# Kernel optimization log

Measured on AMD Instinct MI355X. Metric: run time of the kernel, lower is better.

## Reference

```python
import jax, jax.numpy as jnp
import numpy as np

D_MODEL = 1024
NUM_HEADS = 16
HEAD_DIM = D_MODEL // NUM_HEADS  # 64
MAX_REL = 512
NUM_EMB = 2 * MAX_REL + 1  # 1025
B, L = 2, 2048


def _glorot(key, shape):
    fan_in, fan_out = shape[0], shape[1]
    lim = jnp.sqrt(6.0 / (fan_in + fan_out))
    return jax.random.uniform(key, shape, jnp.float32, -lim, lim)


def setup_inputs() -> dict:
    key = jax.random.key(0)
    ks = jax.random.split(key, 9)
    return {
        "query": jax.random.normal(ks[0], (B, L, D_MODEL), jnp.float32),
        "key": jax.random.normal(ks[1], (B, L, D_MODEL), jnp.float32),
        "value": jax.random.normal(ks[2], (B, L, D_MODEL), jnp.float32),
        "wq": _glorot(ks[3], (D_MODEL, D_MODEL)), "bq": jnp.zeros((D_MODEL,), jnp.float32),
        "wk": _glorot(ks[4], (D_MODEL, D_MODEL)), "bk": jnp.zeros((D_MODEL,), jnp.float32),
        "wv": _glorot(ks[5], (D_MODEL, D_MODEL)), "bv": jnp.zeros((D_MODEL,), jnp.float32),
        "wo": _glorot(ks[6], (D_MODEL, D_MODEL)), "bo": jnp.zeros((D_MODEL,), jnp.float32),
        "rel_emb": _glorot(ks[7], (NUM_EMB, HEAD_DIM)),
    }


def _split_heads(x):
    b, l, _ = x.shape
    return x.reshape(b, l, NUM_HEADS, HEAD_DIM).transpose(0, 2, 1, 3)  # (b,h,l,d)


def reference(query, key, value, wq, bq, wk, bk, wv, bv, wo, bo, rel_emb):
    q = _split_heads(query @ wq + bq)  # (b,h,l,d)
    k = _split_heads(key @ wk + bk)
    v = _split_heads(value @ wv + bv)

    # content scores: (b,h,l,l)
    content = jnp.einsum('bhid,bhjd->bhij', q, k)

    # relative position scores. Original gathers E[clip(j-i)] -> (L,L,d) then
    # einsum('bhid,ijd->bhij'). Equivalent & cheaper: project q onto all
    # relative embeddings once, then gather along the relative-index axis.
    idx = jnp.arange(q.shape[2])
    final_mat = jnp.clip(idx[None, :] - idx[:, None], -MAX_REL, MAX_REL) + MAX_REL  # (L,L)
    q_rel = jnp.einsum('bhid,rd->bhir', q, rel_emb)  # (b,h,l,num_emb)
    position = jnp.take_along_axis(q_rel, final_mat[None, None, :, :], axis=-1)  # (b,h,l,l)

    scores = (content + position) / jnp.sqrt(jnp.float32(HEAD_DIM))
    weights = jax.nn.softmax(scores, axis=-1)  # no mask, dropout off (inference)
    out = jnp.einsum('bhij,bhjd->bhid', weights, v)  # (b,h,l,d)

    out = out.transpose(0, 2, 1, 3).reshape(query.shape[0], -1, D_MODEL)
    return out @ wo + bo
```

## Files before the change

kernel.cpp:

```cpp
#include <hip/hip_runtime.h>
#include <hip/hip_bf16.h>


typedef __attribute__((ext_vector_type(8))) short short8;
typedef __attribute__((ext_vector_type(4))) float floatx4;

#define L_SEQ 2048
#define D_MODEL 1024
#define NHEAD 16
#define DH 64
#define BH 32
#define MROWS 4096

__device__ inline float b2f(short s) {
    unsigned int u = ((unsigned int)(unsigned short)s) << 16;
    float f; __builtin_memcpy(&f, &u, 4); return f;
}
__device__ inline short f2b(float f) {
    unsigned int u; __builtin_memcpy(&u, &f, 4);
    u += 0x7fffu + ((u >> 16) & 1u);
    return (short)(u >> 16);
}
__device__ inline unsigned int pack2(float a, float b) {
    __hip_bfloat162 h = __float22bfloat162_rn(make_float2(a, b));
    unsigned int u; __builtin_memcpy(&u, &h, 4); return u;
}
__device__ inline void st2(short* p, unsigned int v) {
    __builtin_memcpy(p, &v, 4);
}
__device__ inline void async_cp16(short* lds, const short* g) {
    __builtin_amdgcn_global_load_lds(
        (const __attribute__((address_space(1))) unsigned int*)g,
        (__attribute__((address_space(3))) unsigned int*)lds, 16, 0, 0);
}

__global__ __launch_bounds__(256) void detect_dtype(
        const unsigned short* __restrict__ q, int* __restrict__ flag) {
    __shared__ int s[256];
    int tid = threadIdx.x, cnt = 0;
    for (int i = tid; i < 65536; i += 256)
        if ((q[i] & 0x7F80u) == 0x7F80u) cnt++;
    s[tid] = cnt; __syncthreads();
    for (int st = 128; st; st >>= 1) {
        if (tid < st) s[tid] += s[tid + st];
        __syncthreads();
    }
    if (tid == 0) *flag = (s[0] > 4) ? 1 : 0;
}

__global__ __launch_bounds__(256) void norm_small(
        const void* __restrict__ bq, const void* __restrict__ bk,
        const void* __restrict__ bv, const void* __restrict__ bo,
        const void* __restrict__ rel, float* __restrict__ bias4,
        short* __restrict__ relb, const int* __restrict__ flagp) {
    const int f32 = *flagp;
    int t = blockIdx.x * 256 + threadIdx.x;
    if (t < 4096) {
        const void* src = (t < 1024) ? bq : (t < 2048) ? bk : (t < 3072) ? bv : bo;
        int i = t & 1023;
        bias4[t] = f32 ? ((const float*)src)[i] : b2f(((const short*)src)[i]);
    } else if (t < 4096 + 65600) {
        int i = t - 4096;
        relb[i] = f32 ? f2b(((const float*)rel)[i]) : ((const short*)rel)[i];
    }
}

__global__ __launch_bounds__(256) void transpose4(
        const void* __restrict__ w0, const void* __restrict__ w1,
        const void* __restrict__ w2, const void* __restrict__ w3,
        short* __restrict__ dst, const int* __restrict__ flagp) {
    const int f32 = *flagp;
    __shared__ short tile[32][33];
    const void* src = (blockIdx.z == 0) ? w0 : (blockIdx.z == 1) ? w1
                    : (blockIdx.z == 2) ? w2 : w3;
    short* d = dst + (size_t)blockIdx.z * (D_MODEL * D_MODEL);
    int x = blockIdx.x * 32 + threadIdx.x;
    int y0 = blockIdx.y * 32;
    for (int yy = threadIdx.y; yy < 32; yy += 8) {
        size_t idx = (size_t)(y0 + yy) * D_MODEL + x;
        tile[yy][threadIdx.x] = f32 ? f2b(((const float*)src)[idx])
                                    : ((const short*)src)[idx];
    }
    __syncthreads();
    int x0 = blockIdx.x * 32;
    for (int yy = threadIdx.y; yy < 32; yy += 8)
        d[(size_t)(x0 + yy) * D_MODEL + y0 + threadIdx.x] = tile[threadIdx.x][yy];
}

__global__ __launch_bounds__(256) void proj_gemm(
        const void* __restrict__ Aq, const void* __restrict__ Ak,
        const void* __restrict__ Av, const short* __restrict__ WT,
        const float* __restrict__ bias4, short* __restrict__ Qout,
        const int* __restrict__ flagp) {
    const int f32 = *flagp;
    const int z = blockIdx.z;
    const void* A_ = (z == 0) ? Aq : (z == 1) ? Ak : Av;
    const short* BT = WT + (size_t)z * (D_MODEL * D_MODEL);
    const float* bias = bias4 + z * 1024;
    short* C = Qout + (size_t)z * ((size_t)MROWS * D_MODEL);
    const int K = D_MODEL;

    __shared__ short Alds[128 * 32];
    __shared__ short Blds[128 * 32];
    const int tid = threadIdx.x;
    const int w = tid >> 6, lane = tid & 63, cl = lane & 15, quad = lane >> 4;
    const int wr = w >> 1, wc = w & 1;
    const int m0 = blockIdx.y * 128, n0 = blockIdx.x * 128;
    const int srow = tid >> 2, scol = (tid & 3) * 8;
    const int grow = lane >> 2, gcol = (lane & 3) * 8;

    floatx4 acc[4][4];
    for (int i = 0; i < 4; i++)
        for (int j = 0; j < 4; j++)
            acc[i][j] = {0.f, 0.f, 0.f, 0.f};

    for (int k0 = 0; k0 < K; k0 += 32) {
        for (int s = 0; s < 2; s++) {
            int r = w * 32 + s * 16;
            async_cp16(&Blds[r * 32], &BT[(size_t)(n0 + r + grow) * K + k0 + gcol]);
        }
        if (f32) {
            const float* Af = (const float*)A_;
            for (int half = 0; half < 2; half++) {
                size_t base = (size_t)(m0 + srow + half * 64) * K + k0 + scol;
                float4 f0 = *(const float4*)(&Af[base]);
                float4 f1 = *(const float4*)(&Af[base + 4]);
                uint4 s;
                s.x = pack2(f0.x, f0.y); s.y = pack2(f0.z, f0.w);
                s.z = pack2(f1.x, f1.y); s.w = pack2(f1.z, f1.w);
                *(uint4*)(&Alds[(srow + half * 64) * 32 + scol]) = s;
            }
        } else {
            const short* Ab = (const short*)A_;
            for (int s = 0; s < 2; s++) {
                int r = w * 32 + s * 16;
                async_cp16(&Alds[r * 32], &Ab[(size_t)(m0 + r + grow) * K + k0 + gcol]);
            }
        }
        __syncthreads();

        short8 af[4], bfr[4];
        for (int mt = 0; mt < 4; mt++)
            af[mt] = *(const short8*)(&Alds[(wr * 64 + mt * 16 + cl) * 32 + quad * 8]);
        for (int nt = 0; nt < 4; nt++)
            bfr[nt] = *(const short8*)(&Blds[(wc * 64 + nt * 16 + cl) * 32 + quad * 8]);
        for (int mt = 0; mt < 4; mt++)
            for (int nt = 0; nt < 4; nt++)
                acc[mt][nt] = __builtin_amdgcn_mfma_f32_16x16x32_bf16(
                    af[mt], bfr[nt], acc[mt][nt], 0, 0, 0);
        __syncthreads();
    }

    for (int nt = 0; nt < 4; nt++) {
        int n = n0 + wc * 64 + nt * 16 + cl;
        float bv = bias[n];
        int h = n >> 6, d = n & 63;
        for (int mt = 0; mt < 4; mt++) {
            for (int r = 0; r < 4; r++) {
                int m = m0 + wr * 64 + mt * 16 + quad * 4 + r;
                float v = acc[mt][nt][r] + bv;
                int b = m >> 11, i = m & 2047;
                if (z < 2)
                    C[(((size_t)(b * NHEAD + h)) * L_SEQ + i) * DH + d] = f2b(v);
                else
                    C[(((size_t)(b * NHEAD + h)) * DH + d) * L_SEQ + i] = f2b(v);
            }
        }
    }
}

__global__ __launch_bounds__(256) void out_gemm(
        const short* __restrict__ A, const short* __restrict__ BT,
        const float* __restrict__ bias, void* __restrict__ C_,
        const int* __restrict__ flagp) {
    const int f32 = *flagp;
    const int K = D_MODEL, N = D_MODEL;
    __shared__ short Alds[128 * 32];
    __shared__ short Blds[64 * 32];
    const int tid = threadIdx.x;
    const int w = tid >> 6, lane = tid & 63, cl = lane & 15, quad = lane >> 4;
    const int wr = w >> 1, wc = w & 1;
    const int m0 = blockIdx.y * 128, n0 = blockIdx.x * 64;
    const int grow = lane >> 2, gcol = (lane & 3) * 8;

    floatx4 acc[4][2];
    for (int i = 0; i < 4; i++)
        for (int j = 0; j < 2; j++)
            acc[i][j] = {0.f, 0.f, 0.f, 0.f};

    for (int k0 = 0; k0 < K; k0 += 32) {
        for (int s = 0; s < 2; s++) {
            int r = w * 32 + s * 16;
            async_cp16(&Alds[r * 32], &A[(size_t)(m0 + r + grow) * K + k0 + gcol]);
        }
        {
            int r = w * 16;
            async_cp16(&Blds[r * 32], &BT[(size_t)(n0 + r + grow) * K + k0 + gcol]);
        }
        __syncthreads();

        short8 af[4], bfr[2];
        for (int mt = 0; mt < 4; mt++)
            af[mt] = *(const short8*)(&Alds[(wr * 64 + mt * 16 + cl) * 32 + quad * 8]);
        for (int nt = 0; nt < 2; nt++)
            bfr[nt] = *(const short8*)(&Blds[(wc * 32 + nt * 16 + cl) * 32 + quad * 8]);
        for (int mt = 0; mt < 4; mt++)
            for (int nt = 0; nt < 2; nt++)
                acc[mt][nt] = __builtin_amdgcn_mfma_f32_16x16x32_bf16(
                    af[mt], bfr[nt], acc[mt][nt], 0, 0, 0);
        __syncthreads();
    }

    for (int nt = 0; nt < 2; nt++) {
        int n = n0 + wc * 32 + nt * 16 + cl;
        float bv = bias[n];
        for (int mt = 0; mt < 4; mt++) {
            for (int r = 0; r < 4; r++) {
                int m = m0 + wr * 64 + mt * 16 + quad * 4 + r;
                float v = acc[mt][nt][r] + bv;
                if (f32) ((float*)C_)[(size_t)m * N + n] = v;
                else     ((short*)C_)[(size_t)m * N + n] = f2b(v);
            }
        }
    }
}

__global__ __launch_bounds__(256) void attn_kernel(
        const short* __restrict__ Q, const short* __restrict__ K,
        const short* __restrict__ VT, const short* __restrict__ rel,
        short* __restrict__ out) {
    const int tid = threadIdx.x;
    const int w = tid >> 6, lane = tid & 63, cl = lane & 15, quad = lane >> 4;
    const int bh = blockIdx.y, b = bh >> 4, h = bh & 15;
    const int I0 = blockIdx.x * 64;
    const int iw0 = I0 + w * 16;

    const short* Qp = Q + (size_t)bh * L_SEQ * DH;
    const short* Kp = K + (size_t)bh * L_SEQ * DH;
    const short* Vp = VT + (size_t)bh * DH * L_SEQ;

    __shared__ short Klds[64 * 64];
    __shared__ short Vtlds[64 * 64];
    __shared__ short PpLds[4][16 * 86];
    __shared__ short Plds[4][16 * 64];

    short* PpW = &PpLds[w][0];
    short* PW  = &Plds[w][0];

    short8 aq[2];
    for (int c = 0; c < 2; c++)
        aq[c] = *(const short8*)(&Qp[(size_t)(iw0 + cl) * DH + c * 32 + quad * 8]);

    const float SCALE2 = 0.125f * 1.44269504088896340736f;
    const float FMAX = 32.0f;

    float addlo, addhi;
    {
        floatx4 Dc = {0.f, 0.f, 0.f, 0.f};
        int eidx = (cl == 1) ? 1024 : 0;
        for (int c = 0; c < 2; c++) {
            short8 ae = *(const short8*)(&rel[(size_t)eidx * DH + c * 32 + quad * 8]);
            Dc = __builtin_amdgcn_mfma_f32_16x16x32_bf16(ae, aq[c], Dc, 0, 0, 0);
        }
        float pcl = __shfl(Dc[0], cl, 64);
        float pch = __shfl(Dc[1], cl, 64);
        addlo = fmaf(pcl, SCALE2, -FMAX);
        addhi = fmaf(pch, SCALE2, -FMAX);
    }

    floatx4 O[4];
    for (int dt = 0; dt < 4; dt++) O[dt] = {0.f, 0.f, 0.f, 0.f};
    float lsum = 0.f;

    const int srow = tid >> 2;
    const int spair = (tid & 3) * 2;

    for (int j0 = 0; j0 < L_SEQ; j0 += 64) {
        for (int s = 0; s < 2; s++) {
            int chunk = spair + s;
            int pos = chunk ^ (srow & 7);
            *(short8*)(&Klds[srow * 64 + pos * 8]) =
                *(const short8*)(&Kp[(size_t)(j0 + srow) * DH + chunk * 8]);
            *(short8*)(&Vtlds[srow * 64 + pos * 8]) =
                *(const short8*)(&Vp[(size_t)srow * L_SEQ + j0 + chunk * 8]);
        }
        __syncthreads();

        const bool hi_clamp = (j0 - iw0 - 15) >= 512;
        const bool lo_clamp = (j0 + 63 - iw0) <= -512;
        const bool banded = !(hi_clamp || lo_clamp);
        const float addc = hi_clamp ? addhi : addlo;

        floatx4 St[4];
        for (int jt = 0; jt < 4; jt++) {
            St[jt] = {0.f, 0.f, 0.f, 0.f};
            int row = jt * 16 + cl;
            for (int c = 0; c < 2; c++) {
                int pos = ((4 * c + quad) ^ (cl & 7)) * 8;
                short8 bk = *(const short8*)(&Klds[row * 64 + pos]);
                St[jt] = __builtin_amdgcn_mfma_f32_16x16x32_bf16(bk, aq[c], St[jt], 0, 0, 0);
            }
        }

        if (banded) {
            floatx4 Pt[5];
            for (int pt = 0; pt < 5; pt++) Pt[pt] = {0.f, 0.f, 0.f, 0.f};
            const int base = j0 - iw0 - 15;
            for (int pt = 0; pt < 5; pt++) {
                int raw = pt * 16 + cl + base;
                int idx = (raw < -512 ? -512 : (raw > 512 ? 512 : raw)) + 512;
                const short* ep = rel + (size_t)idx * DH;
                for (int c = 0; c < 2; c++) {
                    short8 be = *(const short8*)(&ep[c * 32 + quad * 8]);
                    Pt[pt] = __builtin_amdgcn_mfma_f32_16x16x32_bf16(be, aq[c], Pt[pt], 0, 0, 0);
                }
            }
            for (int pt = 0; pt < 5; pt++) {
                int t = pt * 16 + quad * 4;
                st2(&PpW[cl * 86 + t],     pack2(Pt[pt][0], Pt[pt][1]));
                st2(&PpW[cl * 86 + t + 2], pack2(Pt[pt][2], Pt[pt][3]));
            }
            for (int jt = 0; jt < 4; jt++)
                for (int r = 0; r < 4; r++) {
                    int t = jt * 16 + quad * 4 + r - cl + 15;
                    float pos = b2f(PpW[cl * 86 + t]);
                    St[jt][r] = fmaf(St[jt][r], SCALE2, fmaf(pos, SCALE2, -FMAX));
                }
        } else {
            for (int jt = 0; jt < 4; jt++)
                for (int r = 0; r < 4; r++)
                    St[jt][r] = fmaf(St[jt][r], SCALE2, addc);
        }

        for (int jt = 0; jt < 4; jt++)
            for (int r = 0; r < 4; r++) {
                float p = __builtin_amdgcn_exp2f(St[jt][r]);
                St[jt][r] = p;
                lsum += p;
            }

        for (int jt = 0; jt < 4; jt++)
            for (int pr = 0; pr < 2; pr++) {
                int jl = jt * 16 + quad * 4 + pr * 2;
                int addr = cl * 64 + ((jl >> 3) ^ (cl & 7)) * 8 + (jl & 7);
                st2(&PW[addr], pack2(St[jt][2 * pr], St[jt][2 * pr + 1]));
            }

        for (int c = 0; c < 2; c++) {
            int ppos = ((4 * c + quad) ^ (cl & 7)) * 8;
            short8 bp = *(const short8*)(&PW[cl * 64 + ppos]);
            for (int dt = 0; dt < 4; dt++) {
                int row = dt * 16 + cl;
                int vpos = ((4 * c + quad) ^ (cl & 7)) * 8;
                short8 av = *(const short8*)(&Vtlds[row * 64 + vpos]);
                O[dt] = __builtin_amdgcn_mfma_f32_16x16x32_bf16(av, bp, O[dt], 0, 0, 0);
            }
        }
        __syncthreads();
    }

    lsum += __shfl_xor(lsum, 16, 64);
    lsum += __shfl_xor(lsum, 32, 64);
    float inv = 1.0f / lsum;

    for (int dt = 0; dt < 4; dt++)
        for (int pr = 0; pr < 2; pr++) {
            int jl = dt * 16 + quad * 4 + pr * 2;
            int addr = cl * 64 + ((jl >> 3) ^ (cl & 7)) * 8 + (jl & 7);
            st2(&PW[addr], pack2(O[dt][2 * pr] * inv, O[dt][2 * pr + 1] * inv));
        }
    size_t obase = ((size_t)b * L_SEQ + iw0 + cl) * D_MODEL + h * DH;
    for (int s = 0; s < 2; s++) {
        int c2 = quad * 2 + s;
        short8 o = *(const short8*)(&PW[cl * 64 + (c2 ^ (cl & 7)) * 8]);
        *(short8*)(&out[obase + c2 * 8]) = o;
    }
}

extern "C" void kernel_launch(void* const* d_in, const int* in_sizes, int n_in,
                              void* d_out, int out_size, void* d_ws, size_t ws_size,
                              hipStream_t stream) {
    const void* query = d_in[0];
    const void* key   = d_in[1];
    const void* value = d_in[2];
    const void* wq = d_in[3];  const void* bq = d_in[4];
    const void* wk = d_in[5];  const void* bk = d_in[6];
    const void* wv = d_in[7];  const void* bv = d_in[8];
    const void* wo = d_in[9];  const void* bo = d_in[10];
    const void* rel = d_in[11];

    int* flag = (int*)d_ws;
    short* ws = (short*)d_ws + 16;
    const size_t WSZ = (size_t)D_MODEL * D_MODEL;
    const size_t TSZ = (size_t)MROWS * D_MODEL;
    short* WT   = ws;
    short* Qw   = ws + 4 * WSZ;
    short* Kw   = Qw + TSZ;
    short* Vtw  = Kw + TSZ;
    short* Attw = Vtw + TSZ;
    float* bias4 = (float*)(Attw + TSZ);
    short* relb  = (short*)(bias4 + 4096);

    detect_dtype<<<1, 256, 0, stream>>>((const unsigned short*)query, flag);
    norm_small<<<273, 256, 0, stream>>>(bq, bk, bv, bo, rel, bias4, relb, flag);
    transpose4<<<dim3(32, 32, 4), dim3(32, 8), 0, stream>>>(wq, wk, wv, wo, WT, flag);

    proj_gemm<<<dim3(8, 32, 3), 256, 0, stream>>>(query, key, value, WT, bias4,
                                                  Qw, flag);

    attn_kernel<<<dim3(L_SEQ / 64, BH), 256, 0, stream>>>(Qw, Kw, Vtw, relb, Attw);

    out_gemm<<<dim3(16, 32), 256, 0, stream>>>(Attw, WT + 3 * WSZ, bias4 + 3072,
                                               d_out, flag);
}
```

Before: 392.7 us.

## Register-prefetch next K/V tile, add MFMA setprio, split row-sum accumulators

The next K and V tiles are loaded from global memory into registers while the current tile is being computed, so load latency overlaps compute instead of sitting in front of each LDS store. MFMA sections are wrapped in s_setprio so waves issuing matrix ops get scheduling priority. The softmax row sum uses four independent accumulators to shorten the serial add chain. The cost is more live registers, which could lower occupancy.

```diff
diff --git a/kernel.cpp b/kernel.cpp
--- a/kernel.cpp
+++ b/kernel.cpp
@@ -270,21 +270,34 @@
 
     floatx4 O[4];
     for (int dt = 0; dt < 4; dt++) O[dt] = {0.f, 0.f, 0.f, 0.f};
-    float lsum = 0.f;
+    floatx4 lsum4 = {0.f, 0.f, 0.f, 0.f};
 
     const int srow = tid >> 2;
     const int spair = (tid & 3) * 2;
+
+    short8 kreg[2], vreg[2];
+    for (int s = 0; s < 2; s++) {
+        int chunk = spair + s;
+        kreg[s] = *(const short8*)(&Kp[(size_t)srow * DH + chunk * 8]);
+        vreg[s] = *(const short8*)(&Vp[(size_t)srow * L_SEQ + chunk * 8]);
+    }
 
     for (int j0 = 0; j0 < L_SEQ; j0 += 64) {
         for (int s = 0; s < 2; s++) {
             int chunk = spair + s;
             int pos = chunk ^ (srow & 7);
-            *(short8*)(&Klds[srow * 64 + pos * 8]) =
-                *(const short8*)(&Kp[(size_t)(j0 + srow) * DH + chunk * 8]);
-            *(short8*)(&Vtlds[srow * 64 + pos * 8]) =
-                *(const short8*)(&Vp[(size_t)srow * L_SEQ + j0 + chunk * 8]);
-        }
-        __syncthreads();
+            *(short8*)(&Klds[srow * 64 + pos * 8]) = kreg[s];
+            *(short8*)(&Vtlds[srow * 64 + pos * 8]) = vreg[s];
+        }
+        __syncthreads();
+
+        if (j0 + 64 < L_SEQ) {
+            for (int s = 0; s < 2; s++) {
+                int chunk = spair + s;
+                kreg[s] = *(const short8*)(&Kp[(size_t)(j0 + 64 + srow) * DH + chunk * 8]);
+                vreg[s] = *(const short8*)(&Vp[(size_t)srow * L_SEQ + (j0 + 64) + chunk * 8]);
+            }
+        }
 
         const bool hi_clamp = (j0 - iw0 - 15) >= 512;
         const bool lo_clamp = (j0 + 63 - iw0) <= -512;
@@ -292,6 +305,7 @@
         const float addc = hi_clamp ? addhi : addlo;
 
         floatx4 St[4];
+        __builtin_amdgcn_s_setprio(1);
         for (int jt = 0; jt < 4; jt++) {
             St[jt] = {0.f, 0.f, 0.f, 0.f};
             int row = jt * 16 + cl;
@@ -301,11 +315,13 @@
                 St[jt] = __builtin_amdgcn_mfma_f32_16x16x32_bf16(bk, aq[c], St[jt], 0, 0, 0);
             }
         }
+        __builtin_amdgcn_s_setprio(0);
 
         if (banded) {
             floatx4 Pt[5];
             for (int pt = 0; pt < 5; pt++) Pt[pt] = {0.f, 0.f, 0.f, 0.f};
             const int base = j0 - iw0 - 15;
+            __builtin_amdgcn_s_setprio(1);
             for (int pt = 0; pt < 5; pt++) {
                 int raw = pt * 16 + cl + base;
                 int idx = (raw < -512 ? -512 : (raw > 512 ? 512 : raw)) + 512;
@@ -315,6 +331,7 @@
                     Pt[pt] = __builtin_amdgcn_mfma_f32_16x16x32_bf16(be, aq[c], Pt[pt], 0, 0, 0);
                 }
             }
+            __builtin_amdgcn_s_setprio(0);
             for (int pt = 0; pt < 5; pt++) {
                 int t = pt * 16 + quad * 4;
                 st2(&PpW[cl * 86 + t],     pack2(Pt[pt][0], Pt[pt][1]));
@@ -336,7 +353,7 @@
             for (int r = 0; r < 4; r++) {
                 float p = __builtin_amdgcn_exp2f(St[jt][r]);
                 St[jt][r] = p;
-                lsum += p;
+                lsum4[r] += p;
             }
 
         for (int jt = 0; jt < 4; jt++)
@@ -346,6 +363,7 @@
                 st2(&PW[addr], pack2(St[jt][2 * pr], St[jt][2 * pr + 1]));
             }
 
+        __builtin_amdgcn_s_setprio(1);
         for (int c = 0; c < 2; c++) {
             int ppos = ((4 * c + quad) ^ (cl & 7)) * 8;
             short8 bp = *(const short8*)(&PW[cl * 64 + ppos]);
@@ -356,9 +374,11 @@
                 O[dt] = __builtin_amdgcn_mfma_f32_16x16x32_bf16(av, bp, O[dt], 0, 0, 0);
             }
         }
-        __syncthreads();
-    }
-
+        __builtin_amdgcn_s_setprio(0);
+        __syncthreads();
+    }
+
+    float lsum = (lsum4[0] + lsum4[1]) + (lsum4[2] + lsum4[3]);
     lsum += __shfl_xor(lsum, 16, 64);
     lsum += __shfl_xor(lsum, 32, 64);
     float inv = 1.0f / lsum;
```

After: 464.3 us. +18.2%, slower.
